# Kernel optimization log

Measured on AMD Instinct MI355X. Metric: run time of the kernel, lower is better.

## Reference

```python
import jax, jax.numpy as jnp
import numpy as np

BATCH = 4096
DIM = 512
TEMP = 0.1

def setup_inputs() -> dict:
    key = jax.random.key(0)
    k1, k2 = jax.random.split(key)
    emb_i = jax.random.normal(k1, (BATCH, DIM), dtype=jnp.float32)
    emb_j = jax.random.normal(k2, (BATCH, DIM), dtype=jnp.float32)
    return {"emb_i": emb_i, "emb_j": emb_j}

def _l2_normalize(x, eps=1e-12):
    # matches torch F.normalize(dim=1): x / max(||x||, eps)
    norm = jnp.sqrt(jnp.sum(x * x, axis=1, keepdims=True))
    return x / jnp.maximum(norm, eps)

def reference(emb_i, emb_j):
    n = emb_i.shape[0]
    z_i = _l2_normalize(emb_i)
    z_j = _l2_normalize(emb_j)
    reps = jnp.concatenate([z_i, z_j], axis=0)  # [2N, D], rows unit-norm
    # cosine similarity of unit vectors == dot product -> GEMM instead of O(N^2 D) broadcast
    sim = reps @ reps.T  # [2N, 2N]
    # positives: diag offsets +N and -N
    pos_ij = jnp.sum(z_i * z_j, axis=1)  # diag(sim, +N)
    pos_ji = pos_ij                      # diag(sim, -N) is identical by symmetry
    positives = jnp.concatenate([pos_ij, pos_ji], axis=0)  # [2N]
    nominator = jnp.exp(positives / TEMP)
    neg_mask = 1.0 - jnp.eye(2 * n, dtype=sim.dtype)
    denominator = jnp.sum(neg_mask * jnp.exp(sim / TEMP), axis=1)  # [2N]
    loss_partial = -jnp.log(nominator / denominator)
    return jnp.sum(loss_partial) / (2 * n)
```

## Files before the change

kernel.cpp:

```cpp
#include <hip/hip_runtime.h>
#include <hip/hip_bf16.h>
#include <math.h>

#define N_ROWS 4096
#define DIM    512
#define M_ROWS 8192
#define BK     32
#define NTILES 64
#define NBLOCKS 2080
#define EXP_SCALE 14.4269504088896340736f

typedef unsigned short ushort_t;
typedef __attribute__((ext_vector_type(8))) short short8;
typedef __attribute__((ext_vector_type(4))) float f32x4;

__device__ __forceinline__ ushort_t f2bf(float x) {
  unsigned int bits = __float_as_uint(x);
  unsigned int lsb = (bits >> 16) & 1u;
  bits += 0x7fffu + lsb;
  return (ushort_t)(bits >> 16);
}

__device__ __forceinline__ void store4bf(ushort_t* p, float4 v, float s) {
  union { ushort_t u[4]; uint2 d; } pk;
  pk.u[0] = f2bf(v.x * s);
  pk.u[1] = f2bf(v.y * s);
  pk.u[2] = f2bf(v.z * s);
  pk.u[3] = f2bf(v.w * s);
  *(uint2*)p = pk.d;
}

__device__ __forceinline__ void async16(const ushort_t* g, ushort_t* l) {
  __builtin_amdgcn_global_load_lds(
      (const __attribute__((address_space(1))) void*)g,
      (__attribute__((address_space(3))) void*)l,
      16, 0, 0);
}

__global__ __launch_bounds__(64) void norm_kernel(
    const float* __restrict__ ei, const float* __restrict__ ej,
    ushort_t* __restrict__ reps, float* __restrict__ pos,
    float* __restrict__ denom) {
  int b = blockIdx.x;
  int lane = threadIdx.x;
  if (lane == 0) {
    denom[b] = 0.0f;
    denom[b + N_ROWS] = 0.0f;
  }
  const float4* pi = (const float4*)(ei + (size_t)b * DIM);
  const float4* pj = (const float4*)(ej + (size_t)b * DIM);
  float4 a0 = pi[lane];
  float4 a1 = pi[lane + 64];
  float4 b0 = pj[lane];
  float4 b1 = pj[lane + 64];

  float si = a0.x*a0.x + a0.y*a0.y + a0.z*a0.z + a0.w*a0.w
           + a1.x*a1.x + a1.y*a1.y + a1.z*a1.z + a1.w*a1.w;
  float sj = b0.x*b0.x + b0.y*b0.y + b0.z*b0.z + b0.w*b0.w
           + b1.x*b1.x + b1.y*b1.y + b1.z*b1.z + b1.w*b1.w;
  float dp = a0.x*b0.x + a0.y*b0.y + a0.z*b0.z + a0.w*b0.w
           + a1.x*b1.x + a1.y*b1.y + a1.z*b1.z + a1.w*b1.w;

#pragma unroll
  for (int m = 32; m >= 1; m >>= 1) {
    si += __shfl_xor(si, m, 64);
    sj += __shfl_xor(sj, m, 64);
    dp += __shfl_xor(dp, m, 64);
  }
  float ii = 1.0f / fmaxf(sqrtf(si), 1e-12f);
  float ij = 1.0f / fmaxf(sqrtf(sj), 1e-12f);
  if (lane == 0) pos[b] = dp * ii * ij;

  ushort_t* ri = reps + (size_t)b * DIM;
  ushort_t* rj = reps + (size_t)(b + N_ROWS) * DIM;
  store4bf(ri + lane * 4,       a0, ii);
  store4bf(ri + 256 + lane * 4, a1, ii);
  store4bf(rj + lane * 4,       b0, ij);
  store4bf(rj + 256 + lane * 4, b1, ij);
}

__global__ __launch_bounds__(256) void sim_kernel(
    const ushort_t* __restrict__ reps, float* __restrict__ denom) {
  int id = blockIdx.x;
  id = (id & 7) * (NBLOCKS / 8) + (id >> 3);
  int bj = (int)((sqrtf(8.0f * (float)id + 1.0f) - 1.0f) * 0.5f);
  while ((bj + 1) * (bj + 2) / 2 <= id) ++bj;
  while (bj * (bj + 1) / 2 > id) --bj;
  int bi = id - bj * (bj + 1) / 2;

  __shared__ ushort_t As[2][128 * BK];
  __shared__ ushort_t Bs[2][128 * BK];

  int tid  = threadIdx.x;
  int wave = tid >> 6, lane = tid & 63;
  int wr = wave >> 1, wc = wave & 1;
  int quad = lane >> 4, l15 = lane & 15;

  int c0 = wave * 2, c1 = c0 + 1;
  int srow  = lane >> 2;
  int selem = ((lane & 3) ^ ((srow >> 1) & 3)) * 8;
  const ushort_t* gA0 = reps + (size_t)(bi * 128 + c0 * 16 + srow) * DIM + selem;
  const ushort_t* gA1 = reps + (size_t)(bi * 128 + c1 * 16 + srow) * DIM + selem;
  const ushort_t* gB0 = reps + (size_t)(bj * 128 + c0 * 16 + srow) * DIM + selem;
  const ushort_t* gB1 = reps + (size_t)(bj * 128 + c1 * 16 + srow) * DIM + selem;

  f32x4 zero4 = {0.0f, 0.0f, 0.0f, 0.0f};
  f32x4 acc[4][4];
#pragma unroll
  for (int tr = 0; tr < 4; ++tr)
#pragma unroll
    for (int tc = 0; tc < 4; ++tc) acc[tr][tc] = zero4;

  int sqr = (quad ^ ((l15 >> 1) & 3)) * 8;

  async16(gA0, &As[0][c0 * 512]);
  async16(gA1, &As[0][c1 * 512]);
  async16(gB0, &Bs[0][c0 * 512]);
  async16(gB1, &Bs[0][c1 * 512]);
  __syncthreads();

  int cur = 0;
  for (int kk = 0; kk < DIM; kk += BK) {
    int nxt = cur ^ 1;
    if (kk + BK < DIM) {
      async16(gA0 + kk + BK, &As[nxt][c0 * 512]);
      async16(gA1 + kk + BK, &As[nxt][c1 * 512]);
      async16(gB0 + kk + BK, &Bs[nxt][c0 * 512]);
      async16(gB1 + kk + BK, &Bs[nxt][c1 * 512]);
    }

    short8 aF[4], bF[4];
#pragma unroll
    for (int t = 0; t < 4; ++t) {
      aF[t] = *(const short8*)(&As[cur][(wr * 64 + t * 16 + l15) * BK + sqr]);
      bF[t] = *(const short8*)(&Bs[cur][(wc * 64 + t * 16 + l15) * BK + sqr]);
    }
#pragma unroll
    for (int tr = 0; tr < 4; ++tr)
#pragma unroll
      for (int tc = 0; tc < 4; ++tc)
        acc[tr][tc] = __builtin_amdgcn_mfma_f32_16x16x32_bf16(
            aF[tr], bF[tc], acc[tr][tc], 0, 0, 0);

    __syncthreads();
    cur = nxt;
  }

  int rowg_base = bi * 128 + wr * 64;
  int colg_base = bj * 128 + wc * 64;

  f32x4 rsum[4];
  float csum[4] = {0.0f, 0.0f, 0.0f, 0.0f};
#pragma unroll
  for (int tr = 0; tr < 4; ++tr) rsum[tr] = zero4;

#pragma unroll
  for (int tr = 0; tr < 4; ++tr) {
    int rowg0 = rowg_base + tr * 16 + quad * 4;
#pragma unroll
    for (int tc = 0; tc < 4; ++tc) {
      int colg = colg_base + tc * 16 + l15;
      f32x4 a = acc[tr][tc];
      f32x4 e;
#pragma unroll
      for (int r = 0; r < 4; ++r) {
        float v = exp2f(a[r] * EXP_SCALE);
        e[r] = ((rowg0 + r) == colg) ? 0.0f : v;
      }
      rsum[tr] += e;
      csum[tc] += e[0] + e[1] + e[2] + e[3];
    }
  }

#pragma unroll
  for (int m = 1; m <= 8; m <<= 1)
#pragma unroll
    for (int tr = 0; tr < 4; ++tr)
#pragma unroll
      for (int r = 0; r < 4; ++r)
        rsum[tr][r] += __shfl_xor(rsum[tr][r], m, 64);

  if (l15 == 0) {
#pragma unroll
    for (int tr = 0; tr < 4; ++tr)
#pragma unroll
      for (int r = 0; r < 4; ++r)
        atomicAdd(&denom[rowg_base + tr * 16 + quad * 4 + r], rsum[tr][r]);
  }

  if (bi != bj) {
#pragma unroll
    for (int m = 16; m <= 32; m <<= 1)
#pragma unroll
      for (int tc = 0; tc < 4; ++tc)
        csum[tc] += __shfl_xor(csum[tc], m, 64);
    if (quad == 0) {
#pragma unroll
      for (int tc = 0; tc < 4; ++tc)
        atomicAdd(&denom[colg_base + tc * 16 + l15], csum[tc]);
    }
  }
}

__global__ __launch_bounds__(256) void loss_kernel(
    const float* __restrict__ denom, const float* __restrict__ pos,
    float* __restrict__ out) {
  __shared__ float red[4];
  int tid = threadIdx.x;
  float p = 0.0f;
  for (int r = tid; r < M_ROWS; r += 256)
    p += logf(denom[r]) - pos[r & (N_ROWS - 1)] * 10.0f;
#pragma unroll
  for (int m = 32; m >= 1; m >>= 1) p += __shfl_xor(p, m, 64);
  if ((tid & 63) == 0) red[tid >> 6] = p;
  __syncthreads();
  if (tid == 0)
    out[0] = (red[0] + red[1] + red[2] + red[3]) * (1.0f / M_ROWS);
}

extern "C" void kernel_launch(void* const* d_in, const int* in_sizes, int n_in,
                              void* d_out, int out_size, void* d_ws, size_t ws_size,
                              hipStream_t stream) {
  const float* ei = (const float*)d_in[0];
  const float* ej = (const float*)d_in[1];
  float* out = (float*)d_out;

  char* ws = (char*)d_ws;
  ushort_t* reps = (ushort_t*)ws;
  float* denom = (float*)(ws + (size_t)M_ROWS * DIM * 2);
  float* pos = (float*)(ws + (size_t)M_ROWS * DIM * 2 + M_ROWS * 4);

  norm_kernel<<<N_ROWS, 64, 0, stream>>>(ei, ej, reps, pos, denom);
  sim_kernel<<<NBLOCKS, 256, 0, stream>>>(reps, denom);
  loss_kernel<<<1, 256, 0, stream>>>(denom, pos, out);
}
```

Baseline: 146.2 us.

## Enlarge similarity GEMM tiles to 256x256 with 8 waves and phased MFMA schedule

Moves the symmetric similarity kernel from 128x128 tiles with 4 waves and K-step 32 to 256x256 tiles with 8 waves and K-step 64. Each tile is double-buffered in LDS with XOR-swizzled async global-to-LDS loads. MFMA work is split into four barrier-separated phases with s_setprio around them, and the A-fragment reads are interleaved with the math. The larger tiles are meant to raise operand reuse and cut the number of blocks, global loads and epilogue atomics. The cost is about 128KB of LDS per block, which limits occupancy, and a coarser grid of 528 blocks that may balance unevenly across CUs. The norm kernel now handles four rows per 256-thread block instead of one row per 64-thread block.

```diff
diff --git a/kernel.cpp b/kernel.cpp
--- a/kernel.cpp
+++ b/kernel.cpp
@@ -5,9 +5,9 @@
 #define N_ROWS 4096
 #define DIM    512
 #define M_ROWS 8192
-#define BK     32
-#define NTILES 64
-#define NBLOCKS 2080
+#define NTILE  32
+#define NB     528
+#define NKT    8
 #define EXP_SCALE 14.4269504088896340736f
 
 typedef unsigned short ushort_t;
@@ -37,12 +37,13 @@
       16, 0, 0);
 }
 
-__global__ __launch_bounds__(64) void norm_kernel(
+__global__ __launch_bounds__(256) void norm_kernel(
     const float* __restrict__ ei, const float* __restrict__ ej,
     ushort_t* __restrict__ reps, float* __restrict__ pos,
     float* __restrict__ denom) {
-  int b = blockIdx.x;
-  int lane = threadIdx.x;
+  int wave = threadIdx.x >> 6;
+  int lane = threadIdx.x & 63;
+  int b = blockIdx.x * 4 + wave;
   if (lane == 0) {
     denom[b] = 0.0f;
     denom[b + N_ROWS] = 0.0f;
@@ -79,125 +80,172 @@
   store4bf(rj + 256 + lane * 4, b1, ij);
 }
 
-__global__ __launch_bounds__(256) void sim_kernel(
+__global__ __launch_bounds__(512, 2) void sim_kernel(
     const ushort_t* __restrict__ reps, float* __restrict__ denom) {
   int id = blockIdx.x;
-  id = (id & 7) * (NBLOCKS / 8) + (id >> 3);
+  id = (id & 7) * (NB / 8) + (id >> 3);
   int bj = (int)((sqrtf(8.0f * (float)id + 1.0f) - 1.0f) * 0.5f);
   while ((bj + 1) * (bj + 2) / 2 <= id) ++bj;
   while (bj * (bj + 1) / 2 > id) --bj;
   int bi = id - bj * (bj + 1) / 2;
 
-  __shared__ ushort_t As[2][128 * BK];
-  __shared__ ushort_t Bs[2][128 * BK];
+  __shared__ ushort_t As[2][2][128 * 64];
+  __shared__ ushort_t Bs[2][2][128 * 64];
 
   int tid  = threadIdx.x;
   int wave = tid >> 6, lane = tid & 63;
-  int wr = wave >> 1, wc = wave & 1;
-  int quad = lane >> 4, l15 = lane & 15;
-
-  int c0 = wave * 2, c1 = c0 + 1;
-  int srow  = lane >> 2;
-  int selem = ((lane & 3) ^ ((srow >> 1) & 3)) * 8;
-  const ushort_t* gA0 = reps + (size_t)(bi * 128 + c0 * 16 + srow) * DIM + selem;
-  const ushort_t* gA1 = reps + (size_t)(bi * 128 + c1 * 16 + srow) * DIM + selem;
-  const ushort_t* gB0 = reps + (size_t)(bj * 128 + c0 * 16 + srow) * DIM + selem;
-  const ushort_t* gB1 = reps + (size_t)(bj * 128 + c1 * 16 + srow) * DIM + selem;
+  int wr = wave >> 2, wc = wave & 3;
+  int hb = wc >> 1;
+  int q = lane >> 4, l15 = lane & 15;
+
+  int srow = lane >> 3;
+  int scol = ((lane & 7) ^ srow) * 8;
+  const ushort_t* pA0 = reps + (size_t)(bi * 256 + wave * 8 + srow) * DIM + scol;
+  const ushort_t* pA1 = pA0 + (size_t)128 * DIM;
+  const ushort_t* pB0 = reps + (size_t)(bj * 256 + wave * 8 + srow) * DIM + scol;
+  const ushort_t* pB1 = pB0 + (size_t)128 * DIM;
+
+#define STAGE_TILE(D, KOFF) do {                                   \
+    ushort_t* la0 = &As[D][0][wave * 512];                         \
+    ushort_t* la1 = &As[D][1][wave * 512];                         \
+    ushort_t* lb0 = &Bs[D][0][wave * 512];                         \
+    ushort_t* lb1 = &Bs[D][1][wave * 512];                         \
+    async16(pA0 + (KOFF),            la0);                         \
+    async16(pA0 + 64 * DIM + (KOFF), la0 + 4096);                  \
+    async16(pA1 + (KOFF),            la1);                         \
+    async16(pA1 + 64 * DIM + (KOFF), la1 + 4096);                  \
+    async16(pB0 + (KOFF),            lb0);                         \
+    async16(pB0 + 64 * DIM + (KOFF), lb0 + 4096);                  \
+    async16(pB1 + (KOFF),            lb1);                         \
+    async16(pB1 + 64 * DIM + (KOFF), lb1 + 4096);                  \
+  } while (0)
+
+  int axor = l15 & 7;
+  int aoff0 = l15 * 64 + ((q ^ axor) * 8);
+  int aoff1 = l15 * 64 + (((4 + q) ^ axor) * 8);
+  int boff0 = (wc & 1) * 4096 + aoff0;
+  int boff1 = (wc & 1) * 4096 + aoff1;
 
   f32x4 zero4 = {0.0f, 0.0f, 0.0f, 0.0f};
-  f32x4 acc[4][4];
-#pragma unroll
-  for (int tr = 0; tr < 4; ++tr)
-#pragma unroll
-    for (int tc = 0; tc < 4; ++tc) acc[tr][tc] = zero4;
-
-  int sqr = (quad ^ ((l15 >> 1) & 3)) * 8;
-
-  async16(gA0, &As[0][c0 * 512]);
-  async16(gA1, &As[0][c1 * 512]);
-  async16(gB0, &Bs[0][c0 * 512]);
-  async16(gB1, &Bs[0][c1 * 512]);
-  __syncthreads();
-
-  int cur = 0;
-  for (int kk = 0; kk < DIM; kk += BK) {
-    int nxt = cur ^ 1;
-    if (kk + BK < DIM) {
-      async16(gA0 + kk + BK, &As[nxt][c0 * 512]);
-      async16(gA1 + kk + BK, &As[nxt][c1 * 512]);
-      async16(gB0 + kk + BK, &Bs[nxt][c0 * 512]);
-      async16(gB1 + kk + BK, &Bs[nxt][c1 * 512]);
-    }
-
-    short8 aF[4], bF[4];
-#pragma unroll
-    for (int t = 0; t < 4; ++t) {
-      aF[t] = *(const short8*)(&As[cur][(wr * 64 + t * 16 + l15) * BK + sqr]);
-      bF[t] = *(const short8*)(&Bs[cur][(wc * 64 + t * 16 + l15) * BK + sqr]);
-    }
-#pragma unroll
-    for (int tr = 0; tr < 4; ++tr)
-#pragma unroll
-      for (int tc = 0; tc < 4; ++tc)
-        acc[tr][tc] = __builtin_amdgcn_mfma_f32_16x16x32_bf16(
-            aF[tr], bF[tc], acc[tr][tc], 0, 0, 0);
-
-    __syncthreads();
-    cur = nxt;
-  }
-
-  int rowg_base = bi * 128 + wr * 64;
-  int colg_base = bj * 128 + wc * 64;
-
-  f32x4 rsum[4];
+  f32x4 acc[8][4];
+#pragma unroll
+  for (int m = 0; m < 8; ++m)
+#pragma unroll
+    for (int n = 0; n < 4; ++n) acc[m][n] = zero4;
+
+#define READ_A(DST, MB) do {                                       \
+    DST[0][0] = *(const short8*)(Ah + (MB) * 1024 + aoff0);        \
+    DST[0][1] = *(const short8*)(Ah + (MB) * 1024 + aoff1);        \
+    DST[1][0] = *(const short8*)(Ah + (MB + 1) * 1024 + aoff0);    \
+    DST[1][1] = *(const short8*)(Ah + (MB + 1) * 1024 + aoff1);    \
+  } while (0)
+
+#define MFMA_PH(MB, AF) do {                                                          \
+    _Pragma("unroll")                                                                 \
+    for (int n = 0; n < 4; ++n) {                                                     \
+      acc[MB][n] = __builtin_amdgcn_mfma_f32_16x16x32_bf16(                           \
+          AF[0][0], bfr[0][n], acc[MB][n], 0, 0, 0);                                  \
+      acc[MB][n] = __builtin_amdgcn_mfma_f32_16x16x32_bf16(                           \
+          AF[0][1], bfr[1][n], acc[MB][n], 0, 0, 0);                                  \
+      acc[MB + 1][n] = __builtin_amdgcn_mfma_f32_16x16x32_bf16(                       \
+          AF[1][0], bfr[0][n], acc[MB + 1][n], 0, 0, 0);                              \
+      acc[MB + 1][n] = __builtin_amdgcn_mfma_f32_16x16x32_bf16(                       \
+          AF[1][1], bfr[1][n], acc[MB + 1][n], 0, 0, 0);                              \
+    }                                                                                 \
+  } while (0)
+
+  STAGE_TILE(0, 0);
+  asm volatile("s_waitcnt vmcnt(0)" ::: "memory");
+  __builtin_amdgcn_s_barrier();
+
+  for (int kt = 0; kt < NKT; ++kt) {
+    int cur = kt & 1;
+    const ushort_t* Ah = &As[cur][wr][0];
+    const ushort_t* Bh = &Bs[cur][hb][0];
+
+    if (kt < NKT - 1) STAGE_TILE(cur ^ 1, (kt + 1) * 64);
+
+    short8 bfr[2][4];
+#pragma unroll
+    for (int n = 0; n < 4; ++n) {
+      bfr[0][n] = *(const short8*)(Bh + n * 1024 + boff0);
+      bfr[1][n] = *(const short8*)(Bh + n * 1024 + boff1);
+    }
+    short8 aX[2][2], aY[2][2];
+    READ_A(aX, 0);
+    READ_A(aY, 2);
+
+    __builtin_amdgcn_s_barrier();
+    __builtin_amdgcn_s_setprio(1);
+    MFMA_PH(0, aX);
+    __builtin_amdgcn_s_setprio(0);
+    READ_A(aX, 4);
+
+    __builtin_amdgcn_s_barrier();
+    __builtin_amdgcn_s_setprio(1);
+    MFMA_PH(2, aY);
+    __builtin_amdgcn_s_setprio(0);
+    READ_A(aY, 6);
+
+    __builtin_amdgcn_s_barrier();
+    __builtin_amdgcn_s_setprio(1);
+    MFMA_PH(4, aX);
+    __builtin_amdgcn_s_setprio(0);
+
+    __builtin_amdgcn_s_barrier();
+    __builtin_amdgcn_s_setprio(1);
+    MFMA_PH(6, aY);
+    __builtin_amdgcn_s_setprio(0);
+
+    asm volatile("s_waitcnt vmcnt(0)" ::: "memory");
+    __builtin_amdgcn_s_barrier();
+  }
+
+  int rowb = bi * 256 + wr * 128 + q * 4;
+  int colb = bj * 256 + wc * 64 + l15;
+  bool diag = (bi == bj);
+
+  float rsum[8][4];
   float csum[4] = {0.0f, 0.0f, 0.0f, 0.0f};
 #pragma unroll
-  for (int tr = 0; tr < 4; ++tr) rsum[tr] = zero4;
-
-#pragma unroll
-  for (int tr = 0; tr < 4; ++tr) {
-    int rowg0 = rowg_base + tr * 16 + quad * 4;
-#pragma unroll
-    for (int tc = 0; tc < 4; ++tc) {
-      int colg = colg_base + tc * 16 + l15;
-      f32x4 a = acc[tr][tc];
-      f32x4 e;
+  for (int m = 0; m < 8; ++m)
+#pragma unroll
+    for (int r = 0; r < 4; ++r) rsum[m][r] = 0.0f;
+
+#pragma unroll
+  for (int m = 0; m < 8; ++m) {
+#pragma unroll
+    for (int n = 0; n < 4; ++n) {
+      f32x4 a = acc[m][n];
 #pragma unroll
       for (int r = 0; r < 4; ++r) {
         float v = exp2f(a[r] * EXP_SCALE);
-        e[r] = ((rowg0 + r) == colg) ? 0.0f : v;
+        if (diag && (rowb + m * 16 + r) == (colb + n * 16)) v = 0.0f;
+        rsum[m][r] += v;
+        csum[n] += v;
       }
-      rsum[tr] += e;
-      csum[tc] += e[0] + e[1] + e[2] + e[3];
-    }
-  }
-
-#pragma unroll
-  for (int m = 1; m <= 8; m <<= 1)
-#pragma unroll
-    for (int tr = 0; tr < 4; ++tr)
-#pragma unroll
-      for (int r = 0; r < 4; ++r)
-        rsum[tr][r] += __shfl_xor(rsum[tr][r], m, 64);
-
-  if (l15 == 0) {
-#pragma unroll
-    for (int tr = 0; tr < 4; ++tr)
-#pragma unroll
-      for (int r = 0; r < 4; ++r)
-        atomicAdd(&denom[rowg_base + tr * 16 + quad * 4 + r], rsum[tr][r]);
-  }
-
-  if (bi != bj) {
-#pragma unroll
-    for (int m = 16; m <= 32; m <<= 1)
-#pragma unroll
-      for (int tc = 0; tc < 4; ++tc)
-        csum[tc] += __shfl_xor(csum[tc], m, 64);
-    if (quad == 0) {
-#pragma unroll
-      for (int tc = 0; tc < 4; ++tc)
-        atomicAdd(&denom[colg_base + tc * 16 + l15], csum[tc]);
+    }
+  }
+
+#pragma unroll
+  for (int m = 0; m < 8; ++m)
+#pragma unroll
+    for (int r = 0; r < 4; ++r) {
+      float v = rsum[m][r];
+      v += __shfl_xor(v, 1, 64);
+      v += __shfl_xor(v, 2, 64);
+      v += __shfl_xor(v, 4, 64);
+      v += __shfl_xor(v, 8, 64);
+      if (l15 == 0) atomicAdd(&denom[rowb + m * 16 + r], v);
+    }
+
+  if (!diag) {
+#pragma unroll
+    for (int n = 0; n < 4; ++n) {
+      float v = csum[n];
+      v += __shfl_xor(v, 16, 64);
+      v += __shfl_xor(v, 32, 64);
+      if (q == 0) atomicAdd(&denom[colb + n * 16], v);
     }
   }
 }
@@ -230,7 +278,7 @@
   float* denom = (float*)(ws + (size_t)M_ROWS * DIM * 2);
   float* pos = (float*)(ws + (size_t)M_ROWS * DIM * 2 + M_ROWS * 4);
 
-  norm_kernel<<<N_ROWS, 64, 0, stream>>>(ei, ej, reps, pos, denom);
-  sim_kernel<<<NBLOCKS, 256, 0, stream>>>(reps, denom);
+  norm_kernel<<<N_ROWS / 4, 256, 0, stream>>>(ei, ej, reps, pos, denom);
+  sim_kernel<<<NB, 512, 0, stream>>>(reps, denom);
   loss_kernel<<<1, 256, 0, stream>>>(denom, pos, out);
 }
```

Result: slower. 152.1 us (+4.1%).
